# Optimization experiments

Hardware: AMD Instinct MI355X
Metric: run time of the kernel (lower is better)

## Reference

```python
import jax, jax.numpy as jnp
import numpy as np

LN_EPS = 1e-5

def setup_inputs() -> dict:
    key = jax.random.key(0)
    k1, k2, k3, k4 = jax.random.split(key, 4)
    B, N, D, E = 2, 50000, 128, 800000
    H = jax.random.normal(k1, (B, N, D), dtype=jnp.float32)
    src = jax.random.randint(k2, (E,), 0, N, dtype=jnp.int64)
    dst = jax.random.randint(k3, (E,), 0, N, dtype=jnp.int64)
    W = jax.random.normal(k4, (D, D), dtype=jnp.float32) * (1.0 / np.sqrt(D))
    gamma = jnp.ones((D,), dtype=jnp.float32)
    beta = jnp.zeros((D,), dtype=jnp.float32)
    return {"H": H, "src": src, "dst": dst, "W": W, "gamma": gamma, "beta": beta}

def reference(H, src, dst, W, gamma, beta):
    # m = Linear(H) (no bias): [B,N,D]
    m = jnp.einsum('bnd,de->bne', H, W)
    # gather messages at src, scatter-add into dst along node dim
    agg = jnp.zeros_like(m).at[:, dst, :].add(m[:, src, :])
    x = H + jax.nn.gelu(agg, approximate=False)
    # LayerNorm over last dim
    mu = jnp.mean(x, axis=-1, keepdims=True)
    var = jnp.var(x, axis=-1, keepdims=True)
    return (x - mu) * jax.lax.rsqrt(var + LN_EPS) * gamma + beta
```

## Files before the change

### kernel.cpp

```cpp
#include <hip/hip_runtime.h>
#include <math.h>

#define DIM 128
#define LN_EPS 1e-5f
#define CAP 64
#define TPW 2
#define FBLK 64
#define MAXB 16384

typedef unsigned short bf16_t;
typedef unsigned short u16;
typedef __attribute__((ext_vector_type(8))) short bf16x8;
typedef __attribute__((ext_vector_type(4))) float f32x4;
typedef __attribute__((ext_vector_type(2))) float f32x2;

__device__ __forceinline__ bf16_t f2bf(float f) {
    unsigned u = __builtin_bit_cast(unsigned, f);
    u += 0x7FFFu + ((u >> 16) & 1u);
    return (bf16_t)(u >> 16);
}
__device__ __forceinline__ float lo_bf(unsigned u) {
    return __builtin_bit_cast(float, u << 16);
}
__device__ __forceinline__ float hi_bf(unsigned u) {
    return __builtin_bit_cast(float, u & 0xFFFF0000u);
}

__global__ __launch_bounds__(256) void prep_kernel(
    const float* __restrict__ W, bf16_t* __restrict__ WT)
{
    const int tid = blockIdx.x * 256 + threadIdx.x;
    if (tid < (DIM * DIM / 4)) {
        const float4 w = ((const float4*)W)[tid];
        const int k  = tid >> 5;
        const int n0 = (tid & 31) * 4;
        WT[(n0 + 0) * DIM + k] = f2bf(w.x);
        WT[(n0 + 1) * DIM + k] = f2bf(w.y);
        WT[(n0 + 2) * DIM + k] = f2bf(w.z);
        WT[(n0 + 3) * DIM + k] = f2bf(w.w);
    }
}

__global__ __launch_bounds__(256) void hist_kernel(
    const int* __restrict__ dst, unsigned* __restrict__ hist,
    int bins4, int E, int EPB)
{
    __shared__ unsigned hb[MAXB];
    const int b   = blockIdx.x;
    const int tid = threadIdx.x;
    const int e0  = b * EPB;
    const int e1  = (e0 + EPB < E) ? (e0 + EPB) : E;

    for (int bin0 = 0; bin0 < bins4; bin0 += MAXB) {
        const int nb = (bins4 - bin0 < MAXB) ? (bins4 - bin0) : MAXB;
        for (int i = tid; i < nb; i += 256) hb[i] = 0;
        __syncthreads();
        for (int e = e0 + tid; e < e1; e += 256) {
            const int d   = dst[e];
            const int bin = (d >> 2) - bin0;
            if (bin >= 0 && bin < nb)
                atomicAdd(&hb[bin], 1u << ((d & 3) * 8));
        }
        __syncthreads();
        for (int i = tid; i < nb; i += 256)
            hist[(size_t)b * bins4 + bin0 + i] = hb[i];
        __syncthreads();
    }
}

__global__ __launch_bounds__(256, 2) void scan_gemm_kernel(
    const float* __restrict__ Hmat, const bf16_t* __restrict__ WT,
    bf16_t* __restrict__ Mout,
    const unsigned* __restrict__ hist, unsigned* __restrict__ offs,
    int* __restrict__ cursor,
    int bins4, int N, int nrows, int SB)
{
    if ((int)blockIdx.x < SB) {
        const int bin = blockIdx.x * 256 + threadIdx.x;
        if (bin < bins4) {
            unsigned l0 = 0, l1 = 0, l2 = 0, l3 = 0;
            for (int b = 0; b < FBLK; ++b) {
                const unsigned c = hist[(size_t)b * bins4 + bin];
                offs[(size_t)b * bins4 + bin] =
                    (l0 & 0xFFu) | ((l1 & 0xFFu) << 8) |
                    ((l2 & 0xFFu) << 16) | ((l3 & 0xFFu) << 24);
                l0 += c & 0xFFu;         l1 += (c >> 8) & 0xFFu;
                l2 += (c >> 16) & 0xFFu; l3 += (c >> 24) & 0xFFu;
            }
            const int n = bin * 4;
            if (n     < N) cursor[n]     = (int)l0;
            if (n + 1 < N) cursor[n + 1] = (int)l1;
            if (n + 2 < N) cursor[n + 2] = (int)l2;
            if (n + 3 < N) cursor[n + 3] = (int)l3;
        }
        return;
    }

    const int tid  = threadIdx.x;
    const int wave = tid >> 6;
    const int lane = tid & 63;
    const int quad = lane >> 4;
    const int l15  = lane & 15;

    bf16x8 wf[32];
    #pragma unroll
    for (int t = 0; t < 8; ++t)
        #pragma unroll
        for (int ks = 0; ks < 4; ++ks)
            wf[t * 4 + ks] = *(const bf16x8*)
                &WT[(size_t)(t * 16 + l15) * DIM + ks * 32 + quad * 8];

    const int gblock  = blockIdx.x - SB;
    const int baserow = (gblock * 4 + wave) * (TPW * 16);

    #pragma unroll
    for (int rt = 0; rt < TPW; ++rt) {
        const int arow = baserow + rt * 16 + l15;
        const float* Arow = Hmat + (size_t)((arow < nrows) ? arow : 0) * DIM;

        f32x4 acc[8];
        #pragma unroll
        for (int t = 0; t < 8; ++t) acc[t] = (f32x4){0.f, 0.f, 0.f, 0.f};

        #pragma unroll
        for (int ks = 0; ks < 4; ++ks) {
            const int k0 = ks * 32 + quad * 8;
            float4 a0 = *(const float4*)&Arow[k0];
            float4 a1 = *(const float4*)&Arow[k0 + 4];
            bf16x8 hf;
            hf[0] = (short)f2bf(a0.x); hf[1] = (short)f2bf(a0.y);
            hf[2] = (short)f2bf(a0.z); hf[3] = (short)f2bf(a0.w);
            hf[4] = (short)f2bf(a1.x); hf[5] = (short)f2bf(a1.y);
            hf[6] = (short)f2bf(a1.z); hf[7] = (short)f2bf(a1.w);

            #pragma unroll
            for (int t = 0; t < 8; ++t)
                acc[t] = __builtin_amdgcn_mfma_f32_16x16x32_bf16(
                             wf[t * 4 + ks], hf, acc[t], 0, 0, 0);
        }

        if (arow < nrows) {
            const int b = (arow >= N) ? 1 : 0;
            const int n = arow - (b ? N : 0);
            bf16_t* orow = Mout + ((size_t)n * 2 + b) * DIM;
            #pragma unroll
            for (int t = 0; t < 8; ++t) {
                ushort4 o;
                o.x = f2bf(acc[t][0]); o.y = f2bf(acc[t][1]);
                o.z = f2bf(acc[t][2]); o.w = f2bf(acc[t][3]);
                *(ushort4*)&orow[t * 16 + quad * 4] = o;
            }
        }
    }
}

__global__ __launch_bounds__(256) void scatter_kernel(
    const int* __restrict__ src, const int* __restrict__ dst,
    const unsigned* __restrict__ offs, u16* __restrict__ eidx,
    int bins4, int E, int EPB)
{
    __shared__ unsigned hb[MAXB];
    const int b   = blockIdx.x;
    const int tid = threadIdx.x;
    const int e0  = b * EPB;
    const int e1  = (e0 + EPB < E) ? (e0 + EPB) : E;

    for (int bin0 = 0; bin0 < bins4; bin0 += MAXB) {
        const int nb = (bins4 - bin0 < MAXB) ? (bins4 - bin0) : MAXB;
        for (int i = tid; i < nb; i += 256) hb[i] = 0;
        __syncthreads();
        for (int e = e0 + tid; e < e1; e += 256) {
            const int d   = dst[e];
            const int bin = (d >> 2) - bin0;
            if (bin >= 0 && bin < nb) {
                const int sh = (d & 3) * 8;
                const unsigned old = atomicAdd(&hb[bin], 1u << sh);
                const int rank = (int)((old >> sh) & 0xFFu);
                const int base = (int)((offs[(size_t)b * bins4 + (d >> 2)] >> sh) & 0xFFu);
                const int slot = base + rank;
                if (slot < CAP) eidx[(size_t)d * CAP + slot] = (u16)src[e];
            }
        }
        __syncthreads();
    }
}

__global__ __launch_bounds__(256, 3) void gather_kernel(
    const bf16_t* __restrict__ M, const float* __restrict__ Hmat,
    const int* __restrict__ cursor, const u16* __restrict__ eidx,
    const float* __restrict__ gamma, const float* __restrict__ beta,
    float* __restrict__ out, int N)
{
    const int wave = threadIdx.x >> 6;
    const int lane = threadIdx.x & 63;
    const int node = blockIdx.x * 4 + wave;
    if (node >= N) return;

    const int b  = lane >> 5;
    const int c4 = lane & 31;

    const size_t elembase = ((size_t)b * N + node) * DIM + c4 * 4;
    float4 h  = *(const float4*)&Hmat[elembase];
    float4 gm = *(const float4*)&gamma[c4 * 4];
    float4 bt = *(const float4*)&beta[c4 * 4];

    int cnt = cursor[node];
    if (cnt > CAP) cnt = CAP;

    int myidx = (lane < cnt) ? (int)eidx[(size_t)node * CAP + lane] : 0;

    const uint2* M2 = (const uint2*)M;
    f32x2 accA = {0.f, 0.f}, accB = {0.f, 0.f};

    int j = 0;
    for (; j + 16 <= cnt; j += 16) {
        uint2 v[16];
        #pragma unroll
        for (int q = 0; q < 16; ++q) {
            int s = __builtin_amdgcn_readlane(myidx, j + q);
            v[q] = (M2 + ((size_t)s << 6))[lane];
        }
        __builtin_amdgcn_sched_barrier(0);
        #pragma unroll
        for (int q = 0; q < 16; ++q) {
            accA += (f32x2){ lo_bf(v[q].x), hi_bf(v[q].x) };
            accB += (f32x2){ lo_bf(v[q].y), hi_bf(v[q].y) };
        }
    }
    if (j < cnt) {
        uint2 v[16];
        #pragma unroll
        for (int q = 0; q < 16; ++q) {
            int s = __builtin_amdgcn_readlane(myidx, (j + q) & 63);
            v[q] = (M2 + ((size_t)s << 6))[lane];
        }
        __builtin_amdgcn_sched_barrier(0);
        #pragma unroll
        for (int q = 0; q < 16; ++q) {
            unsigned vx = (j + q < cnt) ? v[q].x : 0u;
            unsigned vy = (j + q < cnt) ? v[q].y : 0u;
            accA += (f32x2){ lo_bf(vx), hi_bf(vx) };
            accB += (f32x2){ lo_bf(vy), hi_bf(vy) };
        }
    }
    float acc0 = accA.x, acc1 = accA.y, acc2 = accB.x, acc3 = accB.y;

    const float inv_sqrt2 = 0.70710678118654752f;
    float x0 = h.x + 0.5f * acc0 * (1.f + erff(acc0 * inv_sqrt2));
    float x1 = h.y + 0.5f * acc1 * (1.f + erff(acc1 * inv_sqrt2));
    float x2 = h.z + 0.5f * acc2 * (1.f + erff(acc2 * inv_sqrt2));
    float x3 = h.w + 0.5f * acc3 * (1.f + erff(acc3 * inv_sqrt2));

    float s  = x0 + x1 + x2 + x3;
    float ss = x0 * x0 + x1 * x1 + x2 * x2 + x3 * x3;
    #pragma unroll
    for (int o = 16; o > 0; o >>= 1) {
        s  += __shfl_xor(s,  o, 64);
        ss += __shfl_xor(ss, o, 64);
    }
    const float mean = s * (1.f / DIM);
    const float var  = ss * (1.f / DIM) - mean * mean;
    const float inv  = rsqrtf(var + LN_EPS);

    float4 o;
    o.x = (x0 - mean) * inv * gm.x + bt.x;
    o.y = (x1 - mean) * inv * gm.y + bt.y;
    o.z = (x2 - mean) * inv * gm.z + bt.z;
    o.w = (x3 - mean) * inv * gm.w + bt.w;
    *(float4*)&out[elembase] = o;
}

extern "C" void kernel_launch(void* const* d_in, const int* in_sizes, int n_in,
                              void* d_out, int out_size, void* d_ws, size_t ws_size,
                              hipStream_t stream)
{
    const float* H     = (const float*)d_in[0];
    const int*   src   = (const int*)  d_in[1];
    const int*   dst   = (const int*)  d_in[2];
    const float* W     = (const float*)d_in[3];
    const float* gamma = (const float*)d_in[4];
    const float* beta  = (const float*)d_in[5];
    float* out = (float*)d_out;

    const int E     = in_sizes[1];
    const int total = in_sizes[0];
    const int nrows = total / DIM;
    const int N     = nrows / 2;

    const int bins4 = (N + 3) / 4;
    const int EPB   = (E + FBLK - 1) / FBLK;

    char* ws = (char*)d_ws;
    bf16_t* Mbuf    = (bf16_t*)ws;   ws += (size_t)total * sizeof(bf16_t);
    int* cursor     = (int*)ws;      ws += (size_t)N * sizeof(int);
    u16* eidx       = (u16*)ws;      ws += (size_t)N * CAP * sizeof(u16);
    bf16_t* WT      = (bf16_t*)ws;   ws += (size_t)DIM * DIM * sizeof(bf16_t);
    unsigned* hist  = (unsigned*)ws; ws += (size_t)FBLK * bins4 * sizeof(unsigned);
    unsigned* offs  = (unsigned*)ws; ws += (size_t)FBLK * bins4 * sizeof(unsigned);

    prep_kernel<<<(DIM * DIM / 4 + 255) / 256, 256, 0, stream>>>(W, WT);

    hist_kernel<<<FBLK, 256, 0, stream>>>(dst, hist, bins4, E, EPB);

    const int SB = (bins4 + 255) / 256;
    const int ROWS_PER_BLOCK = 4 * TPW * 16;
    const int GB = (nrows + ROWS_PER_BLOCK - 1) / ROWS_PER_BLOCK;
    scan_gemm_kernel<<<SB + GB, 256, 0, stream>>>(H, WT, Mbuf, hist, offs,
                                                  cursor, bins4, N, nrows, SB);

    scatter_kernel<<<FBLK, 256, 0, stream>>>(src, dst, offs, eidx, bins4, E, EPB);

    gather_kernel<<<(N + 3) / 4, 256, 0, stream>>>(Mbuf, H, cursor, eidx,
                                                   gamma, beta, out, N);
}
```

Baseline: 277.0 us.

## Regroup kernels so scatter overlaps GEMM and prep merges with histogram

Merges the W transpose/convert prep into the histogram launch, splits the scan into its own small kernel, and co-schedules the edge scatter with the GEMM in one launch so the latency-bound scatter blocks overlap with the compute-bound GEMM blocks. FBLK is doubled to 128, which spreads histogram and scatter work over more blocks. The trade-off is a longer per-bin serial scan and larger hist/offs buffers. The GEMM blocks also now allocate the 64KB shared array, which may reduce their occupancy.

```diff
diff --git a/kernel.cpp b/kernel.cpp
--- a/kernel.cpp
+++ b/kernel.cpp
@@ -5,7 +5,7 @@
 #define LN_EPS 1e-5f
 #define CAP 64
 #define TPW 2
-#define FBLK 64
+#define FBLK 128
 #define MAXB 16384
 
 typedef unsigned short bf16_t;
@@ -26,26 +26,25 @@
     return __builtin_bit_cast(float, u & 0xFFFF0000u);
 }
 
-__global__ __launch_bounds__(256) void prep_kernel(
-    const float* __restrict__ W, bf16_t* __restrict__ WT)
-{
-    const int tid = blockIdx.x * 256 + threadIdx.x;
-    if (tid < (DIM * DIM / 4)) {
-        const float4 w = ((const float4*)W)[tid];
-        const int k  = tid >> 5;
-        const int n0 = (tid & 31) * 4;
-        WT[(n0 + 0) * DIM + k] = f2bf(w.x);
-        WT[(n0 + 1) * DIM + k] = f2bf(w.y);
-        WT[(n0 + 2) * DIM + k] = f2bf(w.z);
-        WT[(n0 + 3) * DIM + k] = f2bf(w.w);
-    }
-}
-
-__global__ __launch_bounds__(256) void hist_kernel(
+__global__ __launch_bounds__(256) void hist_prep_kernel(
     const int* __restrict__ dst, unsigned* __restrict__ hist,
-    int bins4, int E, int EPB)
+    const float* __restrict__ W, bf16_t* __restrict__ WT,
+    int bins4, int E, int EPB, int HB)
 {
     __shared__ unsigned hb[MAXB];
+    if ((int)blockIdx.x >= HB) {
+        const int tid = (blockIdx.x - HB) * 256 + threadIdx.x;
+        if (tid < (DIM * DIM / 4)) {
+            const float4 w = ((const float4*)W)[tid];
+            const int k  = tid >> 5;
+            const int n0 = (tid & 31) * 4;
+            WT[(n0 + 0) * DIM + k] = f2bf(w.x);
+            WT[(n0 + 1) * DIM + k] = f2bf(w.y);
+            WT[(n0 + 2) * DIM + k] = f2bf(w.z);
+            WT[(n0 + 3) * DIM + k] = f2bf(w.w);
+        }
+        return;
+    }
     const int b   = blockIdx.x;
     const int tid = threadIdx.x;
     const int e0  = b * EPB;
@@ -68,30 +67,60 @@
     }
 }
 
-__global__ __launch_bounds__(256, 2) void scan_gemm_kernel(
+__global__ __launch_bounds__(256) void scan_kernel(
+    const unsigned* __restrict__ hist, unsigned* __restrict__ offs,
+    int* __restrict__ cursor, int bins4, int N)
+{
+    const int bin = blockIdx.x * 256 + threadIdx.x;
+    if (bin >= bins4) return;
+    unsigned l0 = 0, l1 = 0, l2 = 0, l3 = 0;
+    for (int b = 0; b < FBLK; ++b) {
+        const unsigned c = hist[(size_t)b * bins4 + bin];
+        offs[(size_t)b * bins4 + bin] =
+            (l0 & 0xFFu) | ((l1 & 0xFFu) << 8) |
+            ((l2 & 0xFFu) << 16) | ((l3 & 0xFFu) << 24);
+        l0 += c & 0xFFu;         l1 += (c >> 8) & 0xFFu;
+        l2 += (c >> 16) & 0xFFu; l3 += (c >> 24) & 0xFFu;
+    }
+    const int n = bin * 4;
+    if (n     < N) cursor[n]     = (int)l0;
+    if (n + 1 < N) cursor[n + 1] = (int)l1;
+    if (n + 2 < N) cursor[n + 2] = (int)l2;
+    if (n + 3 < N) cursor[n + 3] = (int)l3;
+}
+
+__global__ __launch_bounds__(256, 2) void scatter_gemm_kernel(
     const float* __restrict__ Hmat, const bf16_t* __restrict__ WT,
     bf16_t* __restrict__ Mout,
-    const unsigned* __restrict__ hist, unsigned* __restrict__ offs,
-    int* __restrict__ cursor,
-    int bins4, int N, int nrows, int SB)
-{
-    if ((int)blockIdx.x < SB) {
-        const int bin = blockIdx.x * 256 + threadIdx.x;
-        if (bin < bins4) {
-            unsigned l0 = 0, l1 = 0, l2 = 0, l3 = 0;
-            for (int b = 0; b < FBLK; ++b) {
-                const unsigned c = hist[(size_t)b * bins4 + bin];
-                offs[(size_t)b * bins4 + bin] =
-                    (l0 & 0xFFu) | ((l1 & 0xFFu) << 8) |
-                    ((l2 & 0xFFu) << 16) | ((l3 & 0xFFu) << 24);
-                l0 += c & 0xFFu;         l1 += (c >> 8) & 0xFFu;
-                l2 += (c >> 16) & 0xFFu; l3 += (c >> 24) & 0xFFu;
+    const int* __restrict__ src, const int* __restrict__ dst,
+    const unsigned* __restrict__ offs, u16* __restrict__ eidx,
+    int bins4, int nrows, int N, int E, int EPB)
+{
+    __shared__ unsigned hb[MAXB];
+    if ((int)blockIdx.x < FBLK) {
+        const int b   = blockIdx.x;
+        const int tid = threadIdx.x;
+        const int e0  = b * EPB;
+        const int e1  = (e0 + EPB < E) ? (e0 + EPB) : E;
+
+        for (int bin0 = 0; bin0 < bins4; bin0 += MAXB) {
+            const int nb = (bins4 - bin0 < MAXB) ? (bins4 - bin0) : MAXB;
+            for (int i = tid; i < nb; i += 256) hb[i] = 0;
+            __syncthreads();
+            for (int e = e0 + tid; e < e1; e += 256) {
+                const int d   = dst[e];
+                const int bin = (d >> 2) - bin0;
+                if (bin >= 0 && bin < nb) {
+                    const int sh = (d & 3) * 8;
+                    const unsigned old = atomicAdd(&hb[bin], 1u << sh);
+                    const int rank = (int)((old >> sh) & 0xFFu);
+                    const int base =
+                        (int)((offs[(size_t)b * bins4 + (d >> 2)] >> sh) & 0xFFu);
+                    const int slot = base + rank;
+                    if (slot < CAP) eidx[(size_t)d * CAP + slot] = (u16)src[e];
+                }
             }
-            const int n = bin * 4;
-            if (n     < N) cursor[n]     = (int)l0;
-            if (n + 1 < N) cursor[n + 1] = (int)l1;
-            if (n + 2 < N) cursor[n + 2] = (int)l2;
-            if (n + 3 < N) cursor[n + 3] = (int)l3;
+            __syncthreads();
         }
         return;
     }
@@ -110,7 +139,7 @@
             wf[t * 4 + ks] = *(const bf16x8*)
                 &WT[(size_t)(t * 16 + l15) * DIM + ks * 32 + quad * 8];
 
-    const int gblock  = blockIdx.x - SB;
+    const int gblock  = blockIdx.x - FBLK;
     const int baserow = (gblock * 4 + wave) * (TPW * 16);
 
     #pragma unroll
@@ -154,37 +183,6 @@
     }
 }
 
-__global__ __launch_bounds__(256) void scatter_kernel(
-    const int* __restrict__ src, const int* __restrict__ dst,
-    const unsigned* __restrict__ offs, u16* __restrict__ eidx,
-    int bins4, int E, int EPB)
-{
-    __shared__ unsigned hb[MAXB];
-    const int b   = blockIdx.x;
-    const int tid = threadIdx.x;
-    const int e0  = b * EPB;
-    const int e1  = (e0 + EPB < E) ? (e0 + EPB) : E;
-
-    for (int bin0 = 0; bin0 < bins4; bin0 += MAXB) {
-        const int nb = (bins4 - bin0 < MAXB) ? (bins4 - bin0) : MAXB;
-        for (int i = tid; i < nb; i += 256) hb[i] = 0;
-        __syncthreads();
-        for (int e = e0 + tid; e < e1; e += 256) {
-            const int d   = dst[e];
-            const int bin = (d >> 2) - bin0;
-            if (bin >= 0 && bin < nb) {
-                const int sh = (d & 3) * 8;
-                const unsigned old = atomicAdd(&hb[bin], 1u << sh);
-                const int rank = (int)((old >> sh) & 0xFFu);
-                const int base = (int)((offs[(size_t)b * bins4 + (d >> 2)] >> sh) & 0xFFu);
-                const int slot = base + rank;
-                if (slot < CAP) eidx[(size_t)d * CAP + slot] = (u16)src[e];
-            }
-        }
-        __syncthreads();
-    }
-}
-
 __global__ __launch_bounds__(256, 3) void gather_kernel(
     const bf16_t* __restrict__ M, const float* __restrict__ Hmat,
     const int* __restrict__ cursor, const u16* __restrict__ eidx,
@@ -291,24 +289,25 @@
     const int EPB   = (E + FBLK - 1) / FBLK;
 
     char* ws = (char*)d_ws;
-    bf16_t* Mbuf    = (bf16_t*)ws;   ws += (size_t)total * sizeof(bf16_t);
-    int* cursor     = (int*)ws;      ws += (size_t)N * sizeof(int);
-    u16* eidx       = (u16*)ws;      ws += (size_t)N * CAP * sizeof(u16);
-    bf16_t* WT      = (bf16_t*)ws;   ws += (size_t)DIM * DIM * sizeof(bf16_t);
-    unsigned* hist  = (unsigned*)ws; ws += (size_t)FBLK * bins4 * sizeof(unsigned);
-    unsigned* offs  = (unsigned*)ws; ws += (size_t)FBLK * bins4 * sizeof(unsigned);
-
-    prep_kernel<<<(DIM * DIM / 4 + 255) / 256, 256, 0, stream>>>(W, WT);
-
-    hist_kernel<<<FBLK, 256, 0, stream>>>(dst, hist, bins4, E, EPB);
-
-    const int SB = (bins4 + 255) / 256;
+    bf16_t* Mbuf   = (bf16_t*)ws;   ws += (size_t)total * sizeof(bf16_t);
+    int* cursor    = (int*)ws;      ws += (size_t)N * sizeof(int);
+    u16* eidx      = (u16*)ws;      ws += (size_t)N * CAP * sizeof(u16);
+    bf16_t* WT     = (bf16_t*)ws;   ws += (size_t)DIM * DIM * sizeof(bf16_t);
+    unsigned* hist = (unsigned*)ws; ws += (size_t)FBLK * bins4 * sizeof(unsigned);
+    unsigned* offs = (unsigned*)ws; ws += (size_t)FBLK * bins4 * sizeof(unsigned);
+
+    const int PREPB = (DIM * DIM / 4 + 255) / 256;
+    hist_prep_kernel<<<FBLK + PREPB, 256, 0, stream>>>(dst, hist, W, WT,
+                                                       bins4, E, EPB, FBLK);
+
+    scan_kernel<<<(bins4 + 255) / 256, 256, 0, stream>>>(hist, offs, cursor,
+                                                         bins4, N);
+
     const int ROWS_PER_BLOCK = 4 * TPW * 16;
     const int GB = (nrows + ROWS_PER_BLOCK - 1) / ROWS_PER_BLOCK;
-    scan_gemm_kernel<<<SB + GB, 256, 0, stream>>>(H, WT, Mbuf, hist, offs,
-                                                  cursor, bins4, N, nrows, SB);
-
-    scatter_kernel<<<FBLK, 256, 0, stream>>>(src, dst, offs, eidx, bins4, E, EPB);
+    scatter_gemm_kernel<<<FBLK + GB, 256, 0, stream>>>(H, WT, Mbuf, src, dst,
+                                                       offs, eidx, bins4,
+                                                       nrows, N, E, EPB);
 
     gather_kernel<<<(N + 3) / 4, 256, 0, stream>>>(Mbuf, H, cursor, eidx,
                                                    gamma, beta, out, N);
```

Result: faster. 252.3 us (-8.9%).
